# Performance work log

Hardware: AMD Instinct MI355X
Metric: run time of the kernel (lower is better)

The kernel has to match this reference:

```python
import jax, jax.numpy as jnp
import numpy as np

K = 4  # top-k nearest neighbors


def setup_inputs() -> dict:
    key = jax.random.key(0)
    k1, k2, k3 = jax.random.split(key, 3)
    N, D, M = 784, 512, 65536  # N_patches (28*28), feature dim, memory bank size
    query = jax.random.normal(k1, (N, D), dtype=jnp.float32)
    memory_bank = jax.random.normal(k2, (M, D), dtype=jnp.float32)
    # fcn: Conv2d(in=2*D=1024, out=1, kernel=3, padding=1)
    fan_in = 2 * D * 9
    fcn_w = jax.random.normal(k3, (1, 2 * D, 3, 3), dtype=jnp.float32) / np.sqrt(fan_in)
    fcn_b = jnp.zeros((1,), dtype=jnp.float32)
    return {"query": query, "memory_bank": memory_bank, "fcn_w": fcn_w, "fcn_b": fcn_b}


def reference(query, memory_bank, fcn_w, fcn_b):
    # pairwise L2 distances (torch.cdist p=2): [N, M]
    q2 = jnp.sum(query * query, axis=1, keepdims=True)           # [N, 1]
    m2 = jnp.sum(memory_bank * memory_bank, axis=1)              # [M]
    d2 = q2 + m2[None, :] - 2.0 * (query @ memory_bank.T)        # [N, M]
    dist = jnp.sqrt(jnp.maximum(d2, 0.0))
    # top-k smallest distances -> indices
    _, topk_idx = jax.lax.top_k(-dist, K)                        # [N, K]
    neighbors = memory_bank[topk_idx]                            # [N, K, D] gather
    neighbor_mean = jnp.mean(neighbors, axis=1)                  # [N, D]
    combined = jnp.concatenate([query, neighbor_mean], axis=1)   # [N, 2D]
    n, dim = combined.shape
    s = int(np.sqrt(n))                                          # 28
    x = combined.T.reshape(1, dim, s, s)                         # [1, 2D, 28, 28]
    out = jax.lax.conv_general_dilated(
        x, fcn_w, window_strides=(1, 1), padding=((1, 1), (1, 1)),
        dimension_numbers=("NCHW", "OIHW", "NCHW"))
    return out + fcn_b[None, :, None, None]                      # [1, 1, 28, 28]
```

## Files before the change

### kernel.cpp

```cpp
#include <hip/hip_runtime.h>
#include <hip/hip_fp8.h>
#include <stdint.h>

#define DIMS 512
#define NQ 784
#define QPAD 832
#define NTILE 13
#define RESCORE 32
#define CSTR 528
#define TBYTES (64 * CSTR)

typedef float f32x4 __attribute__((ext_vector_type(4)));
typedef long  l2v  __attribute__((ext_vector_type(2)));

__device__ __forceinline__ unsigned umn(unsigned a, unsigned b) { return a < b ? a : b; }
__device__ __forceinline__ unsigned umx(unsigned a, unsigned b) { return a > b ? a : b; }

__device__ __forceinline__ unsigned pk4(float a, float b, float c, float d) {
#if __has_builtin(__builtin_amdgcn_cvt_pk_fp8_f32)
    int v = 0;
    v = __builtin_amdgcn_cvt_pk_fp8_f32(a, b, v, false);
    v = __builtin_amdgcn_cvt_pk_fp8_f32(c, d, v, true);
    return (unsigned)v;
#else
    __hip_fp8_e4m3 x(a), y(b), z(c), w(d);
    return (unsigned)x.__x | ((unsigned)y.__x << 8) | ((unsigned)z.__x << 16) | ((unsigned)w.__x << 24);
#endif
}

__global__ __launch_bounds__(256) void prep_query(const float* __restrict__ q,
                                                  char* __restrict__ qb8p) {
    int gid = blockIdx.x * 256 + threadIdx.x;
    int col = gid >> 6;
    int g = gid & 63;
    float4 a = make_float4(0.f, 0.f, 0.f, 0.f), b = a;
    if (col < NQ) {
        a = *(const float4*)(q + (size_t)col * DIMS + g * 8);
        b = *(const float4*)(q + (size_t)col * DIMS + g * 8 + 4);
    }
    uint2 o;
    o.x = pk4(a.x, a.y, a.z, a.w);
    o.y = pk4(b.x, b.y, b.z, b.w);
    int tile = col >> 6, cin = col & 63;
    *(uint2*)(qb8p + (size_t)tile * TBYTES + cin * CSTR + (g & 3) * 128 + (g >> 2) * 8) = o;
}

__global__ __launch_bounds__(256, 2) void score_kernel(
    const float* __restrict__ bank,
    const char* __restrict__ qb8p,
    uint2* __restrict__ cand)
{
    __shared__ __align__(16) char bt[2][TBYTES];
    __shared__ float m2s[128];

    const int wg = blockIdx.x;
    const int t = threadIdx.x;
    const int v = t >> 6;
    const int lane = t & 63;
    const int lo = lane & 15;
    const int kg = lane >> 4;

#define STAGE(BUF, TILE)                                                              \
    do {                                                                              \
        _Pragma("unroll")                                                             \
        for (int j = 0; j < 8; ++j) {                                                 \
            const int ch = v * 8 + j;                                                 \
            const char* src = qb8p + (size_t)(TILE) * TBYTES + ch * 1024 + lane * 16; \
            __builtin_amdgcn_global_load_lds(                                         \
                (const __attribute__((address_space(1))) unsigned*)src,               \
                (__attribute__((address_space(3))) unsigned*)(&bt[BUF][ch * 1024]),   \
                16, 0, 0);                                                            \
        }                                                                             \
        if (v == 0) {                                                                 \
            const char* src = qb8p + (size_t)(TILE) * TBYTES + 32768 + lane * 16;     \
            __builtin_amdgcn_global_load_lds(                                         \
                (const __attribute__((address_space(1))) unsigned*)src,               \
                (__attribute__((address_space(3))) unsigned*)(&bt[BUF][32768]),       \
                16, 0, 0);                                                            \
        }                                                                             \
    } while (0)

    STAGE(0, 0);

    long areg[2][16];
    float m2p[2];
    #pragma unroll
    for (int m = 0; m < 2; ++m) {
        const float* rp = bank + ((size_t)(wg * 128 + v * 32 + m * 16 + lo)) * DIMS + kg * 8;
        float ss = 0.f;
        #pragma unroll
        for (int ks = 0; ks < 16; ++ks) {
            float4 x = *(const float4*)(rp + ks * 32);
            float4 y = *(const float4*)(rp + ks * 32 + 4);
            ss += x.x * x.x + x.y * x.y + x.z * x.z + x.w * x.w;
            ss += y.x * y.x + y.y * y.y + y.z * y.z + y.w * y.w;
            unsigned l32 = pk4(x.x, x.y, x.z, x.w);
            unsigned h32 = pk4(y.x, y.y, y.z, y.w);
            areg[m][ks] = (long)(((unsigned long long)h32 << 32) | l32);
        }
        m2p[m] = ss;
    }
    #pragma unroll
    for (int m = 0; m < 2; ++m) {
        m2p[m] += __shfl_xor(m2p[m], 16);
        m2p[m] += __shfl_xor(m2p[m], 32);
    }
    if (lane < 16) {
        m2s[v * 32 + lane] = m2p[0];
        m2s[v * 32 + 16 + lane] = m2p[1];
    }

    asm volatile("s_waitcnt vmcnt(0)" ::: "memory");
    __syncthreads();

    f32x4 seed0, seed1;
    #pragma unroll
    for (int j = 0; j < 4; ++j) {
        seed0[j] = -(512.0f + 0.5f * m2s[v * 32 + kg * 4 + j]);
        seed1[j] = -(512.0f + 0.5f * m2s[v * 32 + 16 + kg * 4 + j]);
    }

    const char* pB = &bt[0][0] + lo * CSTR + kg * 128;

#define KSLOOP(ACC, BUF, NTP)                                                              \
    do {                                                                                   \
        __builtin_amdgcn_s_setprio(1);                                                     \
        _Pragma("unroll")                                                                  \
        for (int ks2 = 0; ks2 < 8; ++ks2) {                                                \
            const int off = (BUF) * TBYTES + (NTP) * (32 * CSTR) + ks2 * 16;               \
            l2v B0 = *(const l2v*)(pB + off);                                              \
            l2v B1 = *(const l2v*)(pB + off + 16 * CSTR);                                  \
            ACC[0][0] = __builtin_amdgcn_mfma_f32_16x16x32_fp8_fp8(areg[0][2 * ks2], B0[0], ACC[0][0], 0, 0, 0); \
            ACC[1][0] = __builtin_amdgcn_mfma_f32_16x16x32_fp8_fp8(areg[1][2 * ks2], B0[0], ACC[1][0], 0, 0, 0); \
            ACC[0][1] = __builtin_amdgcn_mfma_f32_16x16x32_fp8_fp8(areg[0][2 * ks2], B1[0], ACC[0][1], 0, 0, 0); \
            ACC[1][1] = __builtin_amdgcn_mfma_f32_16x16x32_fp8_fp8(areg[1][2 * ks2], B1[0], ACC[1][1], 0, 0, 0); \
            ACC[0][0] = __builtin_amdgcn_mfma_f32_16x16x32_fp8_fp8(areg[0][2 * ks2 + 1], B0[1], ACC[0][0], 0, 0, 0); \
            ACC[1][0] = __builtin_amdgcn_mfma_f32_16x16x32_fp8_fp8(areg[1][2 * ks2 + 1], B0[1], ACC[1][0], 0, 0, 0); \
            ACC[0][1] = __builtin_amdgcn_mfma_f32_16x16x32_fp8_fp8(areg[0][2 * ks2 + 1], B1[1], ACC[0][1], 0, 0, 0); \
            ACC[1][1] = __builtin_amdgcn_mfma_f32_16x16x32_fp8_fp8(areg[1][2 * ks2 + 1], B1[1], ACC[1][1], 0, 0, 0); \
        }                                                                                  \
        __builtin_amdgcn_s_setprio(0);                                                     \
    } while (0)

#define SEL(ACC, TILE, NTP)                                                                \
    do {                                                                                   \
        _Pragma("unroll")                                                                  \
        for (int n = 0; n < 2; ++n) {                                                      \
            unsigned v1 = 0xFFFFFFFFu, v2 = 0xFFFFFFFFu;                                   \
            _Pragma("unroll")                                                              \
            for (int m = 0; m < 2; ++m)                                                    \
                _Pragma("unroll")                                                          \
                for (int j = 0; j < 4; ++j) {                                              \
                    unsigned u = ((__float_as_uint(ACC[m][n][j]) ^ 0x80000000u) & ~31u)    \
                                 | (unsigned)(m * 16 + kg * 4 + j);                        \
                    unsigned mx = umx(v1, u);                                              \
                    v1 = umn(v1, u);                                                       \
                    v2 = umn(v2, mx);                                                      \
                }                                                                          \
            _Pragma("unroll")                                                              \
            for (int off = 16; off <= 32; off <<= 1) {                                     \
                unsigned o1 = (unsigned)__shfl_xor((int)v1, off);                          \
                unsigned o2 = (unsigned)__shfl_xor((int)v2, off);                          \
                unsigned mx = umx(v1, o1);                                                 \
                v1 = umn(v1, o1);                                                          \
                v2 = umn(umn(v2, o2), mx);                                                 \
            }                                                                              \
            int col = (TILE) * 64 + (NTP) * 32 + n * 16 + lo;                              \
            if (lane < 16 && col < NQ)                                                     \
                cand[(size_t)(wg * 4 + v) * QPAD + col] = make_uint2(v1, v2);              \
        }                                                                                  \
    } while (0)

#define TILEBODY(TILE, BUF)                                                                \
    do {                                                                                   \
        if ((TILE) + 1 < NTILE) STAGE((BUF) ^ 1, (TILE) + 1);                              \
        f32x4 accP[2][2], accQ[2][2];                                                      \
        accP[0][0] = seed0; accP[0][1] = seed0; accP[1][0] = seed1; accP[1][1] = seed1;    \
        KSLOOP(accP, BUF, 0);                                                              \
        accQ[0][0] = seed0; accQ[0][1] = seed0; accQ[1][0] = seed1; accQ[1][1] = seed1;    \
        KSLOOP(accQ, BUF, 1);                                                              \
        SEL(accP, TILE, 0);                                                                \
        SEL(accQ, TILE, 1);                                                                \
        asm volatile("s_waitcnt vmcnt(0)" ::: "memory");                                   \
        __syncthreads();                                                                   \
    } while (0)

    #pragma unroll 1
    for (int tt = 0; tt < 6; ++tt) {
        TILEBODY(2 * tt, 0);
        TILEBODY(2 * tt + 1, 1);
    }
    TILEBODY(12, 0);

#undef TILEBODY
#undef SEL
#undef KSLOOP
#undef STAGE
}

__global__ __launch_bounds__(256) void merge_kernel(
    const float* __restrict__ query, const float* __restrict__ bank,
    const uint2* __restrict__ cand, float* __restrict__ nm)
{
    __shared__ double d2s[4][32];
    __shared__ int    cis[4][32];

    const int wv = threadIdx.x >> 6, lane = threadIdx.x & 63;
    const int row = blockIdx.x * 4 + wv;

    unsigned s0 = ~0u, s1 = ~0u, s2 = ~0u, s3 = ~0u;
    unsigned s4 = ~0u, s5 = ~0u, s6 = ~0u, s7 = ~0u;

#define INS(U)                                        \
    do {                                              \
        unsigned tt = (U), nv;                        \
        nv = umn(s0, tt); tt = umx(s0, tt); s0 = nv;  \
        nv = umn(s1, tt); tt = umx(s1, tt); s1 = nv;  \
        nv = umn(s2, tt); tt = umx(s2, tt); s2 = nv;  \
        nv = umn(s3, tt); tt = umx(s3, tt); s3 = nv;  \
        nv = umn(s4, tt); tt = umx(s4, tt); s4 = nv;  \
        nv = umn(s5, tt); tt = umx(s5, tt); s5 = nv;  \
        nv = umn(s6, tt); tt = umx(s6, tt); s6 = nv;  \
        s7 = umn(s7, tt);                             \
    } while (0)

    #pragma unroll 4
    for (int j = 0; j < 32; ++j) {
        uint2 e = cand[((size_t)(lane * 32 + j)) * QPAD + row];
        unsigned jb = (unsigned)(j << 5);
        INS((e.x & ~0x3E0u) | jb);
        INS((e.y & ~0x3E0u) | jb);
    }
#undef INS

    const int myC = lane & 31;
    int myCand = 0;
    #pragma unroll
    for (int it = 0; it < RESCORE; ++it) {
        unsigned gm = s0;
        #pragma unroll
        for (int off = 1; off < 64; off <<= 1)
            gm = umn(gm, (unsigned)__shfl_xor((int)gm, off));
        unsigned long long bal = __ballot(s0 == gm);
        int wl = __ffsll((long long)bal) - 1;
        int ci = (wl * 32 + (int)((gm >> 5) & 31u)) * 32 + (int)(gm & 31u);
        myCand = (it == myC) ? ci : myCand;
        if (lane == wl) { s0 = s1; s1 = s2; s2 = s3; s3 = s4; s4 = s5; s5 = s6; s6 = s7; s7 = ~0u; }
    }

    const float* qr = query + (size_t)row * DIMS + (lane >> 5) * 256;
    const float* mr = bank + (size_t)myCand * DIMS + (lane >> 5) * 256;
    double s = 0.0;
    #pragma unroll 8
    for (int i = 0; i < 64; ++i) {
        float4 a = *(const float4*)(qr + i * 4);
        float4 b = *(const float4*)(mr + i * 4);
        double d;
        d = (double)a.x - (double)b.x; s += d * d;
        d = (double)a.y - (double)b.y; s += d * d;
        d = (double)a.z - (double)b.z; s += d * d;
        d = (double)a.w - (double)b.w; s += d * d;
    }
    s += __shfl_xor(s, 32);
    if (lane < 32) { d2s[wv][lane] = s; cis[wv][lane] = myCand; }
    __syncthreads();

    int sel0 = 0, sel1 = 0, sel2 = 0, sel3 = 0;
    unsigned used = 0;
    #pragma unroll
    for (int k = 0; k < 4; ++k) {
        double bv = 1e300; int bidx = 0x7FFFFFFF; int bc = 0;
        for (int c = 0; c < 32; ++c) {
            bool live = !((used >> c) & 1u);
            double dv = d2s[wv][c];
            int cv = cis[wv][c];
            if (live && (dv < bv || (dv == bv && cv < bidx))) { bv = dv; bidx = cv; bc = c; }
        }
        used |= 1u << bc;
        if (k == 0) sel0 = bidx; else if (k == 1) sel1 = bidx;
        else if (k == 2) sel2 = bidx; else sel3 = bidx;
    }

    const float* r0 = bank + (size_t)sel0 * DIMS + lane * 8;
    const float* r1 = bank + (size_t)sel1 * DIMS + lane * 8;
    const float* r2 = bank + (size_t)sel2 * DIMS + lane * 8;
    const float* r3 = bank + (size_t)sel3 * DIMS + lane * 8;
    float* dst = nm + (size_t)row * DIMS + lane * 8;
    #pragma unroll
    for (int h = 0; h < 2; ++h) {
        float4 a = *(const float4*)(r0 + h * 4);
        float4 b = *(const float4*)(r1 + h * 4);
        float4 c = *(const float4*)(r2 + h * 4);
        float4 d = *(const float4*)(r3 + h * 4);
        float4 o;
        o.x = 0.25f * (a.x + b.x + c.x + d.x);
        o.y = 0.25f * (a.y + b.y + c.y + d.y);
        o.z = 0.25f * (a.z + b.z + c.z + d.z);
        o.w = 0.25f * (a.w + b.w + c.w + d.w);
        *(float4*)(dst + h * 4) = o;
    }
}

__global__ __launch_bounds__(256) void conv_kernel(
    const float* __restrict__ query, const float* __restrict__ nm,
    const float* __restrict__ fw, const float* __restrict__ fb,
    float* __restrict__ out)
{
    __shared__ float red[256];
    int pix = blockIdx.x, t = threadIdx.x;
    int i = pix / 28, j = pix % 28;
    float acc = 0.f;
    for (int c = t; c < 1024; c += 256) {
        const float* wrow = fw + c * 9;
        for (int di = 0; di < 3; ++di) {
            int h = i + di - 1;
            if (h < 0 || h >= 28) continue;
            for (int dj = 0; dj < 3; ++dj) {
                int w = j + dj - 1;
                if (w < 0 || w >= 28) continue;
                int n = h * 28 + w;
                float x = (c < 512) ? query[(size_t)n * 512 + c]
                                    : nm[(size_t)n * 512 + (c - 512)];
                acc += x * wrow[di * 3 + dj];
            }
        }
    }
    red[t] = acc;
    __syncthreads();
    for (int s = 128; s; s >>= 1) {
        if (t < s) red[t] += red[t + s];
        __syncthreads();
    }
    if (t == 0) out[pix] = red[0] + fb[0];
}

extern "C" void kernel_launch(void* const* d_in, const int* in_sizes, int n_in,
                              void* d_out, int out_size, void* d_ws, size_t ws_size,
                              hipStream_t stream)
{
    const float* query = (const float*)d_in[0];
    const float* bank  = (const float*)d_in[1];
    const float* fw    = (const float*)d_in[2];
    const float* fb    = (const float*)d_in[3];
    float* out = (float*)d_out;

    char* ws = (char*)d_ws;
    char*  qb8p = ws;
    uint2* cand = (uint2*)(ws + 439296);
    float* nm   = (float*)(ws + 439296 + 13631488);

    prep_query<<<208, 256, 0, stream>>>(query, qb8p);
    score_kernel<<<512, 256, 0, stream>>>(bank, qb8p, cand);
    merge_kernel<<<NQ / 4, 256, 0, stream>>>(query, bank, cand, nm);
    conv_kernel<<<NQ, 256, 0, stream>>>(query, nm, fw, fb, out);
}
```

Measured before the change: 118.3 us.

## Double bank rows per workgroup and split query tiles across two blocks

Each workgroup now holds 256 bank rows (64 per wave, four MFMA row groups) in registers instead of 128. Each block handles only half of the 13 query tiles (tiles 0-6 or 7-12), chosen by a bit of the block index. Each staged query tile is therefore reused across twice as many bank rows, cutting LDS reads per MFMA. The grid shape stays the same while per-block work is rebalanced, at the cost of higher register pressure (areg grows to 4x16 longs) and the bank being converted to fp8 twice per row group.

```diff
diff --git a/kernel.cpp b/kernel.cpp
--- a/kernel.cpp
+++ b/kernel.cpp
@@ -51,42 +51,45 @@
     uint2* __restrict__ cand)
 {
     __shared__ __align__(16) char bt[2][TBYTES];
-    __shared__ float m2s[128];
-
-    const int wg = blockIdx.x;
+    __shared__ float m2s[256];
+
+    const int bid = blockIdx.x;
+    const int wg2 = (bid & 7) | ((bid >> 4) << 3);
+    const int qh  = (bid >> 3) & 1;
+    const int t0 = qh ? 7 : 0;
+    const int t1 = qh ? NTILE : 7;
     const int t = threadIdx.x;
     const int v = t >> 6;
     const int lane = t & 63;
     const int lo = lane & 15;
     const int kg = lane >> 4;
 
-#define STAGE(BUF, TILE)                                                              \
-    do {                                                                              \
-        _Pragma("unroll")                                                             \
-        for (int j = 0; j < 8; ++j) {                                                 \
-            const int ch = v * 8 + j;                                                 \
-            const char* src = qb8p + (size_t)(TILE) * TBYTES + ch * 1024 + lane * 16; \
-            __builtin_amdgcn_global_load_lds(                                         \
-                (const __attribute__((address_space(1))) unsigned*)src,               \
-                (__attribute__((address_space(3))) unsigned*)(&bt[BUF][ch * 1024]),   \
-                16, 0, 0);                                                            \
-        }                                                                             \
-        if (v == 0) {                                                                 \
-            const char* src = qb8p + (size_t)(TILE) * TBYTES + 32768 + lane * 16;     \
-            __builtin_amdgcn_global_load_lds(                                         \
-                (const __attribute__((address_space(1))) unsigned*)src,               \
-                (__attribute__((address_space(3))) unsigned*)(&bt[BUF][32768]),       \
-                16, 0, 0);                                                            \
-        }                                                                             \
+#define STAGE(BUF, TILE)                                                                   \
+    do {                                                                                   \
+        _Pragma("unroll")                                                                  \
+        for (int j = 0; j < 8; ++j) {                                                      \
+            const int ch = v * 8 + j;                                                      \
+            const char* src = qb8p + (size_t)(TILE) * TBYTES + ch * 1024 + lane * 16;      \
+            __builtin_amdgcn_global_load_lds(                                              \
+                (const __attribute__((address_space(1))) unsigned*)src,                    \
+                (__attribute__((address_space(3))) unsigned*)(&bt[0][0] + (BUF) * TBYTES + ch * 1024), \
+                16, 0, 0);                                                                 \
+        }                                                                                  \
+        if (v == 0) {                                                                      \
+            const char* src = qb8p + (size_t)(TILE) * TBYTES + 32768 + lane * 16;          \
+            __builtin_amdgcn_global_load_lds(                                              \
+                (const __attribute__((address_space(1))) unsigned*)src,                    \
+                (__attribute__((address_space(3))) unsigned*)(&bt[0][0] + (BUF) * TBYTES + 32768), \
+                16, 0, 0);                                                                 \
+        }                                                                                  \
     } while (0)
 
-    STAGE(0, 0);
-
-    long areg[2][16];
-    float m2p[2];
-    #pragma unroll
-    for (int m = 0; m < 2; ++m) {
-        const float* rp = bank + ((size_t)(wg * 128 + v * 32 + m * 16 + lo)) * DIMS + kg * 8;
+    STAGE(0, t0);
+
+    long areg[4][16];
+    #pragma unroll
+    for (int m = 0; m < 4; ++m) {
+        const float* rp = bank + ((size_t)(wg2 * 256 + v * 64 + m * 16 + lo)) * DIMS + kg * 8;
         float ss = 0.f;
         #pragma unroll
         for (int ks = 0; ks < 16; ++ks) {
@@ -98,102 +101,94 @@
             unsigned h32 = pk4(y.x, y.y, y.z, y.w);
             areg[m][ks] = (long)(((unsigned long long)h32 << 32) | l32);
         }
-        m2p[m] = ss;
-    }
-    #pragma unroll
-    for (int m = 0; m < 2; ++m) {
-        m2p[m] += __shfl_xor(m2p[m], 16);
-        m2p[m] += __shfl_xor(m2p[m], 32);
-    }
-    if (lane < 16) {
-        m2s[v * 32 + lane] = m2p[0];
-        m2s[v * 32 + 16 + lane] = m2p[1];
+        ss += __shfl_xor(ss, 16);
+        ss += __shfl_xor(ss, 32);
+        if (lane < 16) m2s[v * 64 + m * 16 + lane] = ss;
     }
 
     asm volatile("s_waitcnt vmcnt(0)" ::: "memory");
     __syncthreads();
 
-    f32x4 seed0, seed1;
-    #pragma unroll
-    for (int j = 0; j < 4; ++j) {
-        seed0[j] = -(512.0f + 0.5f * m2s[v * 32 + kg * 4 + j]);
-        seed1[j] = -(512.0f + 0.5f * m2s[v * 32 + 16 + kg * 4 + j]);
-    }
+    f32x4 seed[4];
+    #pragma unroll
+    for (int m = 0; m < 4; ++m)
+        #pragma unroll
+        for (int j = 0; j < 4; ++j)
+            seed[m][j] = -(512.0f + 0.5f * m2s[v * 64 + m * 16 + kg * 4 + j]);
 
     const char* pB = &bt[0][0] + lo * CSTR + kg * 128;
 
-#define KSLOOP(ACC, BUF, NTP)                                                              \
+#define KSLOOP(ACC, PBT, NTP)                                                              \
     do {                                                                                   \
         __builtin_amdgcn_s_setprio(1);                                                     \
         _Pragma("unroll")                                                                  \
         for (int ks2 = 0; ks2 < 8; ++ks2) {                                                \
-            const int off = (BUF) * TBYTES + (NTP) * (32 * CSTR) + ks2 * 16;               \
-            l2v B0 = *(const l2v*)(pB + off);                                              \
-            l2v B1 = *(const l2v*)(pB + off + 16 * CSTR);                                  \
-            ACC[0][0] = __builtin_amdgcn_mfma_f32_16x16x32_fp8_fp8(areg[0][2 * ks2], B0[0], ACC[0][0], 0, 0, 0); \
-            ACC[1][0] = __builtin_amdgcn_mfma_f32_16x16x32_fp8_fp8(areg[1][2 * ks2], B0[0], ACC[1][0], 0, 0, 0); \
-            ACC[0][1] = __builtin_amdgcn_mfma_f32_16x16x32_fp8_fp8(areg[0][2 * ks2], B1[0], ACC[0][1], 0, 0, 0); \
-            ACC[1][1] = __builtin_amdgcn_mfma_f32_16x16x32_fp8_fp8(areg[1][2 * ks2], B1[0], ACC[1][1], 0, 0, 0); \
-            ACC[0][0] = __builtin_amdgcn_mfma_f32_16x16x32_fp8_fp8(areg[0][2 * ks2 + 1], B0[1], ACC[0][0], 0, 0, 0); \
-            ACC[1][0] = __builtin_amdgcn_mfma_f32_16x16x32_fp8_fp8(areg[1][2 * ks2 + 1], B0[1], ACC[1][0], 0, 0, 0); \
-            ACC[0][1] = __builtin_amdgcn_mfma_f32_16x16x32_fp8_fp8(areg[0][2 * ks2 + 1], B1[1], ACC[0][1], 0, 0, 0); \
-            ACC[1][1] = __builtin_amdgcn_mfma_f32_16x16x32_fp8_fp8(areg[1][2 * ks2 + 1], B1[1], ACC[1][1], 0, 0, 0); \
+            const int off = (NTP) * (32 * CSTR) + ks2 * 16;                                \
+            l2v B0 = *(const l2v*)((PBT) + off);                                           \
+            l2v B1 = *(const l2v*)((PBT) + off + 16 * CSTR);                               \
+            _Pragma("unroll")                                                              \
+            for (int m = 0; m < 4; ++m) {                                                  \
+                ACC[m][0] = __builtin_amdgcn_mfma_f32_16x16x32_fp8_fp8(areg[m][2 * ks2], B0[0], ACC[m][0], 0, 0, 0); \
+                ACC[m][1] = __builtin_amdgcn_mfma_f32_16x16x32_fp8_fp8(areg[m][2 * ks2], B1[0], ACC[m][1], 0, 0, 0); \
+            }                                                                              \
+            _Pragma("unroll")                                                              \
+            for (int m = 0; m < 4; ++m) {                                                  \
+                ACC[m][0] = __builtin_amdgcn_mfma_f32_16x16x32_fp8_fp8(areg[m][2 * ks2 + 1], B0[1], ACC[m][0], 0, 0, 0); \
+                ACC[m][1] = __builtin_amdgcn_mfma_f32_16x16x32_fp8_fp8(areg[m][2 * ks2 + 1], B1[1], ACC[m][1], 0, 0, 0); \
+            }                                                                              \
         }                                                                                  \
         __builtin_amdgcn_s_setprio(0);                                                     \
     } while (0)
 
-#define SEL(ACC, TILE, NTP)                                                                \
+#define SEL2(ACC, TILE, NTP)                                                               \
     do {                                                                                   \
         _Pragma("unroll")                                                                  \
-        for (int n = 0; n < 2; ++n) {                                                      \
-            unsigned v1 = 0xFFFFFFFFu, v2 = 0xFFFFFFFFu;                                   \
+        for (int n = 0; n < 2; ++n)                                                        \
             _Pragma("unroll")                                                              \
-            for (int m = 0; m < 2; ++m)                                                    \
+            for (int H = 0; H < 2; ++H) {                                                  \
+                unsigned v1 = 0xFFFFFFFFu, v2 = 0xFFFFFFFFu;                               \
                 _Pragma("unroll")                                                          \
-                for (int j = 0; j < 4; ++j) {                                              \
-                    unsigned u = ((__float_as_uint(ACC[m][n][j]) ^ 0x80000000u) & ~31u)    \
-                                 | (unsigned)(m * 16 + kg * 4 + j);                        \
-                    unsigned mx = umx(v1, u);                                              \
-                    v1 = umn(v1, u);                                                       \
-                    v2 = umn(v2, mx);                                                      \
+                for (int mm = 0; mm < 2; ++mm)                                             \
+                    _Pragma("unroll")                                                      \
+                    for (int j = 0; j < 4; ++j) {                                          \
+                        unsigned u = ((__float_as_uint(ACC[2 * H + mm][n][j]) ^ 0x80000000u) & ~31u) \
+                                     | (unsigned)(mm * 16 + kg * 4 + j);                   \
+                        unsigned mx = umx(v1, u);                                          \
+                        v1 = umn(v1, u);                                                   \
+                        v2 = umn(v2, mx);                                                  \
+                    }                                                                      \
+                _Pragma("unroll")                                                          \
+                for (int off = 16; off <= 32; off <<= 1) {                                 \
+                    unsigned o1 = (unsigned)__shfl_xor((int)v1, off);                      \
+                    unsigned o2 = (unsigned)__shfl_xor((int)v2, off);                      \
+                    unsigned mx = umx(v1, o1);                                             \
+                    v1 = umn(v1, o1);                                                      \
+                    v2 = umn(umn(v2, o2), mx);                                             \
                 }                                                                          \
-            _Pragma("unroll")                                                              \
-            for (int off = 16; off <= 32; off <<= 1) {                                     \
-                unsigned o1 = (unsigned)__shfl_xor((int)v1, off);                          \
-                unsigned o2 = (unsigned)__shfl_xor((int)v2, off);                          \
-                unsigned mx = umx(v1, o1);                                                 \
-                v1 = umn(v1, o1);                                                          \
-                v2 = umn(umn(v2, o2), mx);                                                 \
+                int col = (TILE) * 64 + (NTP) * 32 + n * 16 + lo;                          \
+                if (lane < 16 && col < NQ)                                                 \
+                    cand[(size_t)(wg2 * 8 + v * 2 + H) * QPAD + col] = make_uint2(v1, v2); \
             }                                                                              \
-            int col = (TILE) * 64 + (NTP) * 32 + n * 16 + lo;                              \
-            if (lane < 16 && col < NQ)                                                     \
-                cand[(size_t)(wg * 4 + v) * QPAD + col] = make_uint2(v1, v2);              \
-        }                                                                                  \
     } while (0)
 
-#define TILEBODY(TILE, BUF)                                                                \
-    do {                                                                                   \
-        if ((TILE) + 1 < NTILE) STAGE((BUF) ^ 1, (TILE) + 1);                              \
-        f32x4 accP[2][2], accQ[2][2];                                                      \
-        accP[0][0] = seed0; accP[0][1] = seed0; accP[1][0] = seed1; accP[1][1] = seed1;    \
-        KSLOOP(accP, BUF, 0);                                                              \
-        accQ[0][0] = seed0; accQ[0][1] = seed0; accQ[1][0] = seed1; accQ[1][1] = seed1;    \
-        KSLOOP(accQ, BUF, 1);                                                              \
-        SEL(accP, TILE, 0);                                                                \
-        SEL(accQ, TILE, 1);                                                                \
-        asm volatile("s_waitcnt vmcnt(0)" ::: "memory");                                   \
-        __syncthreads();                                                                   \
-    } while (0)
-
     #pragma unroll 1
-    for (int tt = 0; tt < 6; ++tt) {
-        TILEBODY(2 * tt, 0);
-        TILEBODY(2 * tt + 1, 1);
-    }
-    TILEBODY(12, 0);
-
-#undef TILEBODY
-#undef SEL
+    for (int tile = t0; tile < t1; ++tile) {
+        const int buf = (tile - t0) & 1;
+        if (tile + 1 < t1) STAGE(buf ^ 1, tile + 1);
+        const char* pBt = pB + buf * TBYTES;
+        f32x4 acc[4][2];
+        #pragma unroll
+        for (int m = 0; m < 4; ++m) { acc[m][0] = seed[m]; acc[m][1] = seed[m]; }
+        KSLOOP(acc, pBt, 0);
+        SEL2(acc, tile, 0);
+        #pragma unroll
+        for (int m = 0; m < 4; ++m) { acc[m][0] = seed[m]; acc[m][1] = seed[m]; }
+        KSLOOP(acc, pBt, 1);
+        SEL2(acc, tile, 1);
+        asm volatile("s_waitcnt vmcnt(0)" ::: "memory");
+        __syncthreads();
+    }
+#undef SEL2
 #undef KSLOOP
 #undef STAGE
 }
```

Measured after the change: 188.0 us, median of 3. 58.9% more time.

## Restructure score kernel into 512-thread blocks with 4-deep LDS query pipeline

Applied to the files above, without the earlier changes.

The score kernel now runs 256 blocks of 8 waves, one block per CU, with four LDS buffers for query tiles so loading stays three tiles ahead. Each wave computes a 32x64 output tile per step with 8 accumulators, and the B-fragment LDS reads are double-buffered in registers so they overlap the MFMAs. Barriers are gated by s_waitcnt vmcnt counts instead of draining all loads each tile, which removes the full per-tile drain. The trade-offs are higher register pressure and fewer independent blocks per CU, and correctness depends on the hand-counted outstanding-load numbers.

```diff
diff --git a/kernel.cpp b/kernel.cpp
--- a/kernel.cpp
+++ b/kernel.cpp
@@ -45,13 +45,13 @@
     *(uint2*)(qb8p + (size_t)tile * TBYTES + cin * CSTR + (g & 3) * 128 + (g >> 2) * 8) = o;
 }
 
-__global__ __launch_bounds__(256, 2) void score_kernel(
+__global__ __launch_bounds__(512, 1) void score_kernel(
     const float* __restrict__ bank,
     const char* __restrict__ qb8p,
     uint2* __restrict__ cand)
 {
-    __shared__ __align__(16) char bt[2][TBYTES];
-    __shared__ float m2s[128];
+    __shared__ __align__(16) char bt[4][TBYTES];
+    __shared__ float m2s[256];
 
     const int wg = blockIdx.x;
     const int t = threadIdx.x;
@@ -60,33 +60,34 @@
     const int lo = lane & 15;
     const int kg = lane >> 4;
 
-#define STAGE(BUF, TILE)                                                              \
-    do {                                                                              \
-        _Pragma("unroll")                                                             \
-        for (int j = 0; j < 8; ++j) {                                                 \
-            const int ch = v * 8 + j;                                                 \
-            const char* src = qb8p + (size_t)(TILE) * TBYTES + ch * 1024 + lane * 16; \
-            __builtin_amdgcn_global_load_lds(                                         \
-                (const __attribute__((address_space(1))) unsigned*)src,               \
-                (__attribute__((address_space(3))) unsigned*)(&bt[BUF][ch * 1024]),   \
-                16, 0, 0);                                                            \
-        }                                                                             \
-        if (v == 0) {                                                                 \
-            const char* src = qb8p + (size_t)(TILE) * TBYTES + 32768 + lane * 16;     \
-            __builtin_amdgcn_global_load_lds(                                         \
-                (const __attribute__((address_space(1))) unsigned*)src,               \
-                (__attribute__((address_space(3))) unsigned*)(&bt[BUF][32768]),       \
-                16, 0, 0);                                                            \
-        }                                                                             \
+#define STAGE(BUF, TILE)                                                                   \
+    do {                                                                                   \
+        if (v == 7) {                                                                      \
+            const char* s32 = qb8p + (size_t)(TILE) * TBYTES + 32 * 1024 + lane * 16;      \
+            __builtin_amdgcn_global_load_lds(                                              \
+                (const __attribute__((address_space(1))) unsigned*)s32,                    \
+                (__attribute__((address_space(3))) unsigned*)(&bt[0][0] + (size_t)(BUF) * TBYTES + 32 * 1024), \
+                16, 0, 0);                                                                 \
+        }                                                                                  \
+        _Pragma("unroll")                                                                  \
+        for (int j = 0; j < 4; ++j) {                                                      \
+            const int ch = v * 4 + j;                                                      \
+            const char* src = qb8p + (size_t)(TILE) * TBYTES + ch * 1024 + lane * 16;      \
+            __builtin_amdgcn_global_load_lds(                                              \
+                (const __attribute__((address_space(1))) unsigned*)src,                    \
+                (__attribute__((address_space(3))) unsigned*)(&bt[0][0] + (size_t)(BUF) * TBYTES + ch * 1024), \
+                16, 0, 0);                                                                 \
+        }                                                                                  \
     } while (0)
 
     STAGE(0, 0);
+    STAGE(1, 1);
+    STAGE(2, 2);
 
     long areg[2][16];
-    float m2p[2];
     #pragma unroll
     for (int m = 0; m < 2; ++m) {
-        const float* rp = bank + ((size_t)(wg * 128 + v * 32 + m * 16 + lo)) * DIMS + kg * 8;
+        const float* rp = bank + ((size_t)(wg * 256 + v * 32 + m * 16 + lo)) * DIMS + kg * 8;
         float ss = 0.f;
         #pragma unroll
         for (int ks = 0; ks < 16; ++ks) {
@@ -98,60 +99,58 @@
             unsigned h32 = pk4(y.x, y.y, y.z, y.w);
             areg[m][ks] = (long)(((unsigned long long)h32 << 32) | l32);
         }
-        m2p[m] = ss;
-    }
-    #pragma unroll
-    for (int m = 0; m < 2; ++m) {
-        m2p[m] += __shfl_xor(m2p[m], 16);
-        m2p[m] += __shfl_xor(m2p[m], 32);
-    }
-    if (lane < 16) {
-        m2s[v * 32 + lane] = m2p[0];
-        m2s[v * 32 + 16 + lane] = m2p[1];
-    }
-
-    asm volatile("s_waitcnt vmcnt(0)" ::: "memory");
-    __syncthreads();
-
-    f32x4 seed0, seed1;
-    #pragma unroll
-    for (int j = 0; j < 4; ++j) {
-        seed0[j] = -(512.0f + 0.5f * m2s[v * 32 + kg * 4 + j]);
-        seed1[j] = -(512.0f + 0.5f * m2s[v * 32 + 16 + kg * 4 + j]);
-    }
+        ss += __shfl_xor(ss, 16);
+        ss += __shfl_xor(ss, 32);
+        if (lane < 16) m2s[v * 32 + m * 16 + lane] = ss;
+    }
+
+    f32x4 seed[2];
+    #pragma unroll
+    for (int m = 0; m < 2; ++m)
+        #pragma unroll
+        for (int j = 0; j < 4; ++j)
+            seed[m][j] = -(512.0f + 0.5f * m2s[v * 32 + m * 16 + kg * 4 + j]);
 
     const char* pB = &bt[0][0] + lo * CSTR + kg * 128;
 
-#define KSLOOP(ACC, BUF, NTP)                                                              \
-    do {                                                                                   \
-        __builtin_amdgcn_s_setprio(1);                                                     \
-        _Pragma("unroll")                                                                  \
-        for (int ks2 = 0; ks2 < 8; ++ks2) {                                                \
-            const int off = (BUF) * TBYTES + (NTP) * (32 * CSTR) + ks2 * 16;               \
-            l2v B0 = *(const l2v*)(pB + off);                                              \
-            l2v B1 = *(const l2v*)(pB + off + 16 * CSTR);                                  \
-            ACC[0][0] = __builtin_amdgcn_mfma_f32_16x16x32_fp8_fp8(areg[0][2 * ks2], B0[0], ACC[0][0], 0, 0, 0); \
-            ACC[1][0] = __builtin_amdgcn_mfma_f32_16x16x32_fp8_fp8(areg[1][2 * ks2], B0[0], ACC[1][0], 0, 0, 0); \
-            ACC[0][1] = __builtin_amdgcn_mfma_f32_16x16x32_fp8_fp8(areg[0][2 * ks2], B1[0], ACC[0][1], 0, 0, 0); \
-            ACC[1][1] = __builtin_amdgcn_mfma_f32_16x16x32_fp8_fp8(areg[1][2 * ks2], B1[0], ACC[1][1], 0, 0, 0); \
-            ACC[0][0] = __builtin_amdgcn_mfma_f32_16x16x32_fp8_fp8(areg[0][2 * ks2 + 1], B0[1], ACC[0][0], 0, 0, 0); \
-            ACC[1][0] = __builtin_amdgcn_mfma_f32_16x16x32_fp8_fp8(areg[1][2 * ks2 + 1], B0[1], ACC[1][0], 0, 0, 0); \
-            ACC[0][1] = __builtin_amdgcn_mfma_f32_16x16x32_fp8_fp8(areg[0][2 * ks2 + 1], B1[1], ACC[0][1], 0, 0, 0); \
-            ACC[1][1] = __builtin_amdgcn_mfma_f32_16x16x32_fp8_fp8(areg[1][2 * ks2 + 1], B1[1], ACC[1][1], 0, 0, 0); \
-        }                                                                                  \
-        __builtin_amdgcn_s_setprio(0);                                                     \
-    } while (0)
-
-#define SEL(ACC, TILE, NTP)                                                                \
+#define LOADB(DST, PBT, KS2)                                       \
+    do {                                                           \
+        DST##0 = *(const l2v*)((PBT) + 0 * 8448 + (KS2) * 16);     \
+        DST##1 = *(const l2v*)((PBT) + 1 * 8448 + (KS2) * 16);     \
+        DST##2 = *(const l2v*)((PBT) + 2 * 8448 + (KS2) * 16);     \
+        DST##3 = *(const l2v*)((PBT) + 3 * 8448 + (KS2) * 16);     \
+    } while (0)
+
+#define MFMAS(B, KS2)                                                                            \
+    do {                                                                                         \
+        acc[0][0] = __builtin_amdgcn_mfma_f32_16x16x32_fp8_fp8(areg[0][2*(KS2)], B##0[0], acc[0][0], 0, 0, 0); \
+        acc[1][0] = __builtin_amdgcn_mfma_f32_16x16x32_fp8_fp8(areg[1][2*(KS2)], B##0[0], acc[1][0], 0, 0, 0); \
+        acc[0][1] = __builtin_amdgcn_mfma_f32_16x16x32_fp8_fp8(areg[0][2*(KS2)], B##1[0], acc[0][1], 0, 0, 0); \
+        acc[1][1] = __builtin_amdgcn_mfma_f32_16x16x32_fp8_fp8(areg[1][2*(KS2)], B##1[0], acc[1][1], 0, 0, 0); \
+        acc[0][2] = __builtin_amdgcn_mfma_f32_16x16x32_fp8_fp8(areg[0][2*(KS2)], B##2[0], acc[0][2], 0, 0, 0); \
+        acc[1][2] = __builtin_amdgcn_mfma_f32_16x16x32_fp8_fp8(areg[1][2*(KS2)], B##2[0], acc[1][2], 0, 0, 0); \
+        acc[0][3] = __builtin_amdgcn_mfma_f32_16x16x32_fp8_fp8(areg[0][2*(KS2)], B##3[0], acc[0][3], 0, 0, 0); \
+        acc[1][3] = __builtin_amdgcn_mfma_f32_16x16x32_fp8_fp8(areg[1][2*(KS2)], B##3[0], acc[1][3], 0, 0, 0); \
+        acc[0][0] = __builtin_amdgcn_mfma_f32_16x16x32_fp8_fp8(areg[0][2*(KS2)+1], B##0[1], acc[0][0], 0, 0, 0); \
+        acc[1][0] = __builtin_amdgcn_mfma_f32_16x16x32_fp8_fp8(areg[1][2*(KS2)+1], B##0[1], acc[1][0], 0, 0, 0); \
+        acc[0][1] = __builtin_amdgcn_mfma_f32_16x16x32_fp8_fp8(areg[0][2*(KS2)+1], B##1[1], acc[0][1], 0, 0, 0); \
+        acc[1][1] = __builtin_amdgcn_mfma_f32_16x16x32_fp8_fp8(areg[1][2*(KS2)+1], B##1[1], acc[1][1], 0, 0, 0); \
+        acc[0][2] = __builtin_amdgcn_mfma_f32_16x16x32_fp8_fp8(areg[0][2*(KS2)+1], B##2[1], acc[0][2], 0, 0, 0); \
+        acc[1][2] = __builtin_amdgcn_mfma_f32_16x16x32_fp8_fp8(areg[1][2*(KS2)+1], B##2[1], acc[1][2], 0, 0, 0); \
+        acc[0][3] = __builtin_amdgcn_mfma_f32_16x16x32_fp8_fp8(areg[0][2*(KS2)+1], B##3[1], acc[0][3], 0, 0, 0); \
+        acc[1][3] = __builtin_amdgcn_mfma_f32_16x16x32_fp8_fp8(areg[1][2*(KS2)+1], B##3[1], acc[1][3], 0, 0, 0); \
+    } while (0)
+
+#define SELT(T)                                                                            \
     do {                                                                                   \
         _Pragma("unroll")                                                                  \
-        for (int n = 0; n < 2; ++n) {                                                      \
+        for (int n = 0; n < 4; ++n) {                                                      \
             unsigned v1 = 0xFFFFFFFFu, v2 = 0xFFFFFFFFu;                                   \
             _Pragma("unroll")                                                              \
             for (int m = 0; m < 2; ++m)                                                    \
                 _Pragma("unroll")                                                          \
                 for (int j = 0; j < 4; ++j) {                                              \
-                    unsigned u = ((__float_as_uint(ACC[m][n][j]) ^ 0x80000000u) & ~31u)    \
+                    unsigned u = ((__float_as_uint(acc[m][n][j]) ^ 0x80000000u) & ~31u)    \
                                  | (unsigned)(m * 16 + kg * 4 + j);                        \
                     unsigned mx = umx(v1, u);                                              \
                     v1 = umn(v1, u);                                                       \
@@ -165,36 +164,53 @@
                 v1 = umn(v1, o1);                                                          \
                 v2 = umn(umn(v2, o2), mx);                                                 \
             }                                                                              \
-            int col = (TILE) * 64 + (NTP) * 32 + n * 16 + lo;                              \
+            int col = (T) * 64 + n * 16 + lo;                                              \
             if (lane < 16 && col < NQ)                                                     \
-                cand[(size_t)(wg * 4 + v) * QPAD + col] = make_uint2(v1, v2);              \
+                cand[(size_t)(wg * 8 + v) * QPAD + col] = make_uint2(v1, v2);              \
         }                                                                                  \
     } while (0)
 
-#define TILEBODY(TILE, BUF)                                                                \
+#define COMPUTE(T)                                                                         \
     do {                                                                                   \
-        if ((TILE) + 1 < NTILE) STAGE((BUF) ^ 1, (TILE) + 1);                              \
-        f32x4 accP[2][2], accQ[2][2];                                                      \
-        accP[0][0] = seed0; accP[0][1] = seed0; accP[1][0] = seed1; accP[1][1] = seed1;    \
-        KSLOOP(accP, BUF, 0);                                                              \
-        accQ[0][0] = seed0; accQ[0][1] = seed0; accQ[1][0] = seed1; accQ[1][1] = seed1;    \
-        KSLOOP(accQ, BUF, 1);                                                              \
-        SEL(accP, TILE, 0);                                                                \
-        SEL(accQ, TILE, 1);                                                                \
-        asm volatile("s_waitcnt vmcnt(0)" ::: "memory");                                   \
-        __syncthreads();                                                                   \
-    } while (0)
+        const char* pBt = pB + (size_t)((T) & 3) * TBYTES;                                 \
+        f32x4 acc[2][4];                                                                   \
+        _Pragma("unroll")                                                                  \
+        for (int m = 0; m < 2; ++m)                                                        \
+            _Pragma("unroll")                                                              \
+            for (int n = 0; n < 4; ++n) acc[m][n] = seed[m];                               \
+        l2v Ba0, Ba1, Ba2, Ba3, Bb0, Bb1, Bb2, Bb3;                                        \
+        LOADB(Ba, pBt, 0);                                                                 \
+        __builtin_amdgcn_s_setprio(1);                                                     \
+        LOADB(Bb, pBt, 1); MFMAS(Ba, 0);                                                   \
+        LOADB(Ba, pBt, 2); MFMAS(Bb, 1);                                                   \
+        LOADB(Bb, pBt, 3); MFMAS(Ba, 2);                                                   \
+        LOADB(Ba, pBt, 4); MFMAS(Bb, 3);                                                   \
+        LOADB(Bb, pBt, 5); MFMAS(Ba, 4);                                                   \
+        LOADB(Ba, pBt, 6); MFMAS(Bb, 5);                                                   \
+        LOADB(Bb, pBt, 7); MFMAS(Ba, 6);                                                   \
+        MFMAS(Bb, 7);                                                                      \
+        __builtin_amdgcn_s_setprio(0);                                                     \
+        SELT(T);                                                                           \
+    } while (0)
+
+#define WAITV(N) asm volatile("s_waitcnt vmcnt(" #N ")" ::: "memory")
 
     #pragma unroll 1
-    for (int tt = 0; tt < 6; ++tt) {
-        TILEBODY(2 * tt, 0);
-        TILEBODY(2 * tt + 1, 1);
-    }
-    TILEBODY(12, 0);
-
-#undef TILEBODY
-#undef SEL
-#undef KSLOOP
+    for (int tile = 0; tile < 10; ++tile) {
+        WAITV(8);
+        __builtin_amdgcn_s_barrier();
+        STAGE((tile + 3) & 3, tile + 3);
+        COMPUTE(tile);
+    }
+    WAITV(8);  __builtin_amdgcn_s_barrier();  COMPUTE(10);
+    WAITV(4);  __builtin_amdgcn_s_barrier();  COMPUTE(11);
+    WAITV(0);  __builtin_amdgcn_s_barrier();  COMPUTE(12);
+
+#undef WAITV
+#undef COMPUTE
+#undef SELT
+#undef MFMAS
+#undef LOADB
 #undef STAGE
 }
 
@@ -350,7 +366,7 @@
     float* nm   = (float*)(ws + 439296 + 13631488);
 
     prep_query<<<208, 256, 0, stream>>>(query, qb8p);
-    score_kernel<<<512, 256, 0, stream>>>(bank, qb8p, cand);
+    score_kernel<<<256, 512, 0, stream>>>(bank, qb8p, cand);
     merge_kernel<<<NQ / 4, 256, 0, stream>>>(query, bank, cand, nm);
     conv_kernel<<<NQ, 256, 0, stream>>>(query, nm, fw, fb, out);
 }
```

Result: slower. 121.0 us (+2.3%).
